# Performance work log

Hardware: AMD Instinct MI355X
Metric: run time of the kernel (lower is better)

## Reference

```python
import jax, jax.numpy as jnp
import numpy as np

NUM_NODES = 100000
NUM_EDGES = 1600000
EMBED_DIM = 128
NUM_CLASSES = 2
NUM_LAYERS = 3


def setup_inputs() -> dict:
    key = jax.random.key(0)
    k_row, k_col, k_val, k_emb, k_a, k_w, k_b = jax.random.split(key, 7)
    node_indices = jnp.arange(NUM_NODES, dtype=jnp.int64 if jax.config.read('jax_enable_x64') else jnp.int32)
    adj_row = jax.random.randint(k_row, (NUM_EDGES,), 0, NUM_NODES)
    adj_col = jax.random.randint(k_col, (NUM_EDGES,), 0, NUM_NODES)
    # symmetric-normalized-ish positive edge weights
    adj_val = jax.random.uniform(k_val, (NUM_EDGES,), dtype=jnp.float32) * (1.0 / 16.0)
    embedding = jax.random.normal(k_emb, (NUM_NODES, EMBED_DIM), dtype=jnp.float32)
    alpha = jnp.ones((NUM_LAYERS + 1,), dtype=jnp.float32) / (NUM_LAYERS + 1)
    W = jax.random.normal(k_w, (EMBED_DIM, NUM_CLASSES), dtype=jnp.float32) * 0.05
    b = jnp.zeros((NUM_CLASSES,), dtype=jnp.float32)
    return {
        'node_indices': node_indices, 'adj_row': adj_row, 'adj_col': adj_col,
        'adj_val': adj_val, 'embedding': embedding, 'alpha': alpha, 'W': W, 'b': b,
    }


def reference(node_indices, adj_row, adj_col, adj_val, embedding, alpha, W, b):
    # x: [N, D] embedding lookup
    x = embedding[node_indices]
    a = jax.nn.softmax(alpha)
    # alpha-weighted running sum over propagation layers (dropout in eval mode = identity)
    acc = a[0] * x
    cur = x
    for i in range(NUM_LAYERS):
        # sparse SpMM: out[r] += val * cur[c] for each edge (r, c)
        msgs = adj_val[:, None] * cur[adj_col]          # [E, D]
        cur = jax.ops.segment_sum(msgs, adj_row, num_segments=NUM_NODES)
        acc = acc + a[i + 1] * cur
    return acc @ W + b  # [N, num_classes]
```

## Files before the change

### kernel.cpp

```cpp
#include <hip/hip_runtime.h>

#define GD(x,y) (((x)+(y)-1)/(y))

#define SH    10
#define BPR   (1 << SH)
#define BS    256
#define KSPL  24
#define CAPSH 15
#define CAP   (1 << CAPSH)
#define CHUNK 2048

static __device__ __forceinline__ float2 ntload2(const float2* p){
    unsigned long long u = __builtin_nontemporal_load((const unsigned long long*)p);
    return *(float2*)&u;
}
static __device__ __forceinline__ void ntstore2(float2* p, float2 v){
    __builtin_nontemporal_store(*(unsigned long long*)&v, (unsigned long long*)p);
}

__global__ void init_k(int* __restrict__ cursor, int NBK,
                       const float* __restrict__ alpha, float* __restrict__ a, int na){
    int t = threadIdx.x;
    if (t < NBK) cursor[t] = t << CAPSH;
    if (t == 0){
        float m = alpha[0];
        for (int i = 1; i < na; ++i) m = fmaxf(m, alpha[i]);
        float s = 0.f;
        for (int i = 0; i < na; ++i){ float e = expf(alpha[i] - m); a[i] = e; s += e; }
        float inv = 1.f / s;
        for (int i = 0; i < na; ++i) a[i] *= inv;
    }
}

__global__ void fillf_k(const int* __restrict__ row, const int* __restrict__ col,
                        const float* __restrict__ val, int* __restrict__ cursor,
                        int2* __restrict__ sep, int E, int NBK){
    __shared__ int2 staged[CHUNK];
    __shared__ unsigned char bid[CHUNK];
    __shared__ int h[128], lstart[128], gbase[128], lcur[128];
    int t = threadIdx.x;
    int s = blockIdx.x * CHUNK;
    int e = min(E, s + CHUNK);
    int cnt = e - s;
    for (int i = t; i < NBK; i += BS) h[i] = 0;
    __syncthreads();
    for (int base = s + t * 4; base < e; base += BS * 4){
        if (base + 3 < e){
            int4 r4 = *(const int4*)(row + base);
            atomicAdd(&h[r4.x >> SH], 1);
            atomicAdd(&h[r4.y >> SH], 1);
            atomicAdd(&h[r4.z >> SH], 1);
            atomicAdd(&h[r4.w >> SH], 1);
        } else {
            for (int j = 0; j < 4 && base + j < e; ++j)
                atomicAdd(&h[row[base + j] >> SH], 1);
        }
    }
    __syncthreads();
    if (t == 0){
        int run = 0;
        for (int i = 0; i < NBK; ++i){ lstart[i] = run; run += h[i]; }
    }
    __syncthreads();
    if (t < NBK){
        lcur[t] = lstart[t];
        gbase[t] = (h[t] > 0) ? atomicAdd(&cursor[t], h[t]) : 0;
    }
    __syncthreads();
    for (int base = s + t * 4; base < e; base += BS * 4){
        int  r[4]; int c[4]; float v[4];
        int  m = min(4, e - base);
        if (m == 4){
            int4 r4 = *(const int4*)(row + base);
            int4 c4 = *(const int4*)(col + base);
            float4 v4 = *(const float4*)(val + base);
            r[0]=r4.x; r[1]=r4.y; r[2]=r4.z; r[3]=r4.w;
            c[0]=c4.x; c[1]=c4.y; c[2]=c4.z; c[3]=c4.w;
            v[0]=v4.x; v[1]=v4.y; v[2]=v4.z; v[3]=v4.w;
        } else {
            for (int j = 0; j < m; ++j){ r[j]=row[base+j]; c[j]=col[base+j]; v[j]=val[base+j]; }
        }
        for (int j = 0; j < m; ++j){
            int b = r[j] >> SH;
            int lp = atomicAdd(&lcur[b], 1);
            int2 pk;
            pk.x = c[j] | ((r[j] & (BPR - 1)) << 17);
            pk.y = __float_as_int(v[j]);
            staged[lp] = pk;
            bid[lp] = (unsigned char)b;
        }
    }
    __syncthreads();
    for (int idx = t; idx < cnt; idx += BS){
        int b = bid[idx];
        sep[gbase[b] + (idx - lstart[b])] = staged[idx];
    }
}

__global__ void proj_k(const float* __restrict__ emb, const int* __restrict__ idx,
                       const float* __restrict__ W, const float* __restrict__ b,
                       const float* __restrict__ a, float* __restrict__ y,
                       float* __restrict__ out, int N){
    int t = blockIdx.x * blockDim.x + threadIdx.x;
    int w = t >> 6;
    int lane = t & 63;
    int n = w * 2 + (lane >> 5);
    if (n >= N) return;
    int sl = lane & 31;
    float4 x = ((const float4*)(emb + (size_t)idx[n] * 128))[sl];
    int d0 = 4 * sl;
    float s0 = x.x * W[d0*2]   + x.y * W[d0*2+2] + x.z * W[d0*2+4] + x.w * W[d0*2+6];
    float s1 = x.x * W[d0*2+1] + x.y * W[d0*2+3] + x.z * W[d0*2+5] + x.w * W[d0*2+7];
    #pragma unroll
    for (int off = 16; off; off >>= 1){
        s0 += __shfl_down(s0, off, 32);
        s1 += __shfl_down(s1, off, 32);
    }
    if (sl == 0){
        float c = a[0];
        ((float2*)y)[n]   = make_float2(s0, s1);
        ((float2*)out)[n] = make_float2(b[0] + c * s0, b[1] + c * s1);
    }
}

__global__ void spmm_k(const int* __restrict__ cursor, const int2* __restrict__ sep,
                       const float* __restrict__ yin, float* __restrict__ partial,
                       int NBK){
    __shared__ float accx[BPR];
    __shared__ float accy[BPR];
    int b  = blockIdx.x / KSPL;
    int sp = blockIdx.x % KSPL;
    int t  = threadIdx.x;
    for (int j = t; j < BPR; j += BS){ accx[j] = 0.f; accy[j] = 0.f; }
    __syncthreads();
    int s = b << CAPSH;
    int e = cursor[b];
    int len = e - s, per = GD(len, KSPL);
    int cs = s + sp * per, ce = min(e, cs + per);
    int i = cs + t;
    for (; i + 3 * BS < ce; i += 4 * BS){
        int2 p0 = sep[i], p1 = sep[i + BS], p2 = sep[i + 2*BS], p3 = sep[i + 3*BS];
        float2 m0 = ((const float2*)yin)[p0.x & 0x1FFFF];
        float2 m1 = ((const float2*)yin)[p1.x & 0x1FFFF];
        float2 m2 = ((const float2*)yin)[p2.x & 0x1FFFF];
        float2 m3 = ((const float2*)yin)[p3.x & 0x1FFFF];
        float v0 = __int_as_float(p0.y), v1 = __int_as_float(p1.y);
        float v2 = __int_as_float(p2.y), v3 = __int_as_float(p3.y);
        atomicAdd(&accx[p0.x >> 17], v0 * m0.x); atomicAdd(&accy[p0.x >> 17], v0 * m0.y);
        atomicAdd(&accx[p1.x >> 17], v1 * m1.x); atomicAdd(&accy[p1.x >> 17], v1 * m1.y);
        atomicAdd(&accx[p2.x >> 17], v2 * m2.x); atomicAdd(&accy[p2.x >> 17], v2 * m2.y);
        atomicAdd(&accx[p3.x >> 17], v3 * m3.x); atomicAdd(&accy[p3.x >> 17], v3 * m3.y);
    }
    for (; i < ce; i += BS){
        int2 pk = sep[i];
        float v = __int_as_float(pk.y);
        float2 m = ((const float2*)yin)[pk.x & 0x1FFFF];
        atomicAdd(&accx[pk.x >> 17], v * m.x);
        atomicAdd(&accy[pk.x >> 17], v * m.y);
    }
    __syncthreads();
    float2* dst = (float2*)partial + (size_t)(b * KSPL + sp) * BPR;
    for (int j = t; j < BPR; j += BS)
        ntstore2(&dst[j], make_float2(accx[j], accy[j]));
}

__global__ void comb_k(const float* __restrict__ partial, const float* __restrict__ a,
                       int ai, float* __restrict__ ynext, float* __restrict__ out,
                       int N, int store){
    int n = blockIdx.x * blockDim.x + threadIdx.x;
    if (n >= N) return;
    int b = n >> SH, j = n & (BPR - 1);
    const float2* p = (const float2*)partial + (size_t)b * KSPL * BPR + j;
    float sx = 0.f, sy = 0.f;
    #pragma unroll
    for (int sp = 0; sp < KSPL; ++sp){
        float2 v = ntload2(&p[(size_t)sp * BPR]);
        sx += v.x; sy += v.y;
    }
    if (store) ((float2*)ynext)[n] = make_float2(sx, sy);
    float c = a[ai];
    float2 o = ((float2*)out)[n];
    o.x += c * sx; o.y += c * sy;
    ((float2*)out)[n] = o;
}

extern "C" void kernel_launch(void* const* d_in, const int* in_sizes, int n_in,
                              void* d_out, int out_size, void* d_ws, size_t ws_size,
                              hipStream_t stream) {
    const int*   node_idx = (const int*)  d_in[0];
    const int*   adj_row  = (const int*)  d_in[1];
    const int*   adj_col  = (const int*)  d_in[2];
    const float* adj_val  = (const float*)d_in[3];
    const float* emb      = (const float*)d_in[4];
    const float* alpha    = (const float*)d_in[5];
    const float* W        = (const float*)d_in[6];
    const float* b        = (const float*)d_in[7];
    float* out = (float*)d_out;

    const int N = in_sizes[0];
    const int E = in_sizes[1];
    const int L = in_sizes[5] - 1;
    const int NBK = GD(N, BPR);
    const int GF  = GD(E, CHUNK);

    char* w = (char*)d_ws;
    float* yA     = (float*)w;  w += (size_t)N * 2 * 4;
    float* yB     = (float*)w;  w += (size_t)N * 2 * 4;
    float* partial= (float*)w;  w += (size_t)NBK * KSPL * BPR * 2 * 4;
    int2*  sep    = (int2*)w;   w += (size_t)NBK * CAP * 8;
    int*   cursor = (int*)w;    w += 1024;
    float* a      = (float*)w;

    init_k<<<1, 128, 0, stream>>>(cursor, NBK, alpha, a, L + 1);
    fillf_k<<<GF, BS, 0, stream>>>(adj_row, adj_col, adj_val, cursor, sep, E, NBK);

    proj_k<<<GD(N * 32, 256), 256, 0, stream>>>(emb, node_idx, W, b, a, yA, out, N);

    float* ysrc = yA;
    float* ydst = yB;
    for (int i = 0; i < L; ++i){
        spmm_k<<<NBK * KSPL, BS, 0, stream>>>(cursor, sep, ysrc, partial, NBK);
        comb_k<<<GD(N, 256), 256, 0, stream>>>(partial, a, i + 1, ydst, out,
                                               N, (i < L - 1) ? 1 : 0);
        float* tmp = ysrc; ysrc = ydst; ydst = tmp;
    }
}
```

Before: 125.8 us.

## Fuse edge bucketing with projection kernel, parallelize scan, batch SpMM gathers

The edge-bucketing kernel and the embedding-projection kernel now run in one launch, split by block index, so the two independent stages can overlap and one launch is saved. The single-thread serial prefix sum over bucket histograms becomes a 128-wide shared-memory Hillis-Steele scan. In the SpMM kernel each thread first loads up to four packed edges, then issues all of their gathers before the atomics. This raises memory-level parallelism for the short per-thread edge counts, where the old 4-way unrolled loop rarely ran. The fused kernel carries the larger shared-memory footprint into the projection blocks, which may limit their occupancy.

After: 218.7 us. 73.8% more time.

```diff
diff --git a/kernel.cpp b/kernel.cpp
--- a/kernel.cpp
+++ b/kernel.cpp
@@ -32,94 +32,102 @@
     }
 }
 
-__global__ void fillf_k(const int* __restrict__ row, const int* __restrict__ col,
-                        const float* __restrict__ val, int* __restrict__ cursor,
-                        int2* __restrict__ sep, int E, int NBK){
-    __shared__ int2 staged[CHUNK];
-    __shared__ unsigned char bid[CHUNK];
-    __shared__ int h[128], lstart[128], gbase[128], lcur[128];
-    int t = threadIdx.x;
-    int s = blockIdx.x * CHUNK;
-    int e = min(E, s + CHUNK);
-    int cnt = e - s;
-    for (int i = t; i < NBK; i += BS) h[i] = 0;
-    __syncthreads();
-    for (int base = s + t * 4; base < e; base += BS * 4){
-        if (base + 3 < e){
-            int4 r4 = *(const int4*)(row + base);
-            atomicAdd(&h[r4.x >> SH], 1);
-            atomicAdd(&h[r4.y >> SH], 1);
-            atomicAdd(&h[r4.z >> SH], 1);
-            atomicAdd(&h[r4.w >> SH], 1);
-        } else {
-            for (int j = 0; j < 4 && base + j < e; ++j)
-                atomicAdd(&h[row[base + j] >> SH], 1);
-        }
-    }
-    __syncthreads();
-    if (t == 0){
-        int run = 0;
-        for (int i = 0; i < NBK; ++i){ lstart[i] = run; run += h[i]; }
-    }
-    __syncthreads();
-    if (t < NBK){
-        lcur[t] = lstart[t];
-        gbase[t] = (h[t] > 0) ? atomicAdd(&cursor[t], h[t]) : 0;
-    }
-    __syncthreads();
-    for (int base = s + t * 4; base < e; base += BS * 4){
-        int  r[4]; int c[4]; float v[4];
-        int  m = min(4, e - base);
-        if (m == 4){
-            int4 r4 = *(const int4*)(row + base);
-            int4 c4 = *(const int4*)(col + base);
-            float4 v4 = *(const float4*)(val + base);
-            r[0]=r4.x; r[1]=r4.y; r[2]=r4.z; r[3]=r4.w;
-            c[0]=c4.x; c[1]=c4.y; c[2]=c4.z; c[3]=c4.w;
-            v[0]=v4.x; v[1]=v4.y; v[2]=v4.z; v[3]=v4.w;
-        } else {
-            for (int j = 0; j < m; ++j){ r[j]=row[base+j]; c[j]=col[base+j]; v[j]=val[base+j]; }
-        }
-        for (int j = 0; j < m; ++j){
-            int b = r[j] >> SH;
-            int lp = atomicAdd(&lcur[b], 1);
-            int2 pk;
-            pk.x = c[j] | ((r[j] & (BPR - 1)) << 17);
-            pk.y = __float_as_int(v[j]);
-            staged[lp] = pk;
-            bid[lp] = (unsigned char)b;
-        }
-    }
-    __syncthreads();
-    for (int idx = t; idx < cnt; idx += BS){
-        int b = bid[idx];
-        sep[gbase[b] + (idx - lstart[b])] = staged[idx];
-    }
-}
-
-__global__ void proj_k(const float* __restrict__ emb, const int* __restrict__ idx,
-                       const float* __restrict__ W, const float* __restrict__ b,
-                       const float* __restrict__ a, float* __restrict__ y,
-                       float* __restrict__ out, int N){
-    int t = blockIdx.x * blockDim.x + threadIdx.x;
-    int w = t >> 6;
-    int lane = t & 63;
-    int n = w * 2 + (lane >> 5);
-    if (n >= N) return;
-    int sl = lane & 31;
-    float4 x = ((const float4*)(emb + (size_t)idx[n] * 128))[sl];
-    int d0 = 4 * sl;
-    float s0 = x.x * W[d0*2]   + x.y * W[d0*2+2] + x.z * W[d0*2+4] + x.w * W[d0*2+6];
-    float s1 = x.x * W[d0*2+1] + x.y * W[d0*2+3] + x.z * W[d0*2+5] + x.w * W[d0*2+7];
-    #pragma unroll
-    for (int off = 16; off; off >>= 1){
-        s0 += __shfl_down(s0, off, 32);
-        s1 += __shfl_down(s1, off, 32);
-    }
-    if (sl == 0){
-        float c = a[0];
-        ((float2*)y)[n]   = make_float2(s0, s1);
-        ((float2*)out)[n] = make_float2(b[0] + c * s0, b[1] + c * s1);
+__global__ void fillproj_k(const int* __restrict__ row, const int* __restrict__ col,
+                           const float* __restrict__ val, int* __restrict__ cursor,
+                           int2* __restrict__ sep, int E, int NBK, int GF,
+                           const float* __restrict__ emb, const int* __restrict__ idx,
+                           const float* __restrict__ W, const float* __restrict__ bb,
+                           const float* __restrict__ a, float* __restrict__ y,
+                           float* __restrict__ out, int N){
+    if (blockIdx.x < GF){
+        __shared__ int2 staged[CHUNK];
+        __shared__ unsigned char bid[CHUNK];
+        __shared__ int h[128], sc[128], lstart[128], gbase[128], lcur[128];
+        int t = threadIdx.x;
+        int s = blockIdx.x * CHUNK;
+        int e = min(E, s + CHUNK);
+        int cnt = e - s;
+        if (t < 128) h[t] = 0;
+        __syncthreads();
+        for (int base = s + t * 4; base < e; base += BS * 4){
+            if (base + 3 < e){
+                int4 r4 = *(const int4*)(row + base);
+                atomicAdd(&h[r4.x >> SH], 1);
+                atomicAdd(&h[r4.y >> SH], 1);
+                atomicAdd(&h[r4.z >> SH], 1);
+                atomicAdd(&h[r4.w >> SH], 1);
+            } else {
+                for (int j = 0; j < 4 && base + j < e; ++j)
+                    atomicAdd(&h[row[base + j] >> SH], 1);
+            }
+        }
+        __syncthreads();
+        int v = (t < 128) ? h[t] : 0;
+        if (t < 128) sc[t] = v;
+        __syncthreads();
+        #pragma unroll
+        for (int off = 1; off < 128; off <<= 1){
+            int add = (t < 128 && t >= off) ? sc[t - off] : 0;
+            __syncthreads();
+            if (t < 128) sc[t] += add;
+            __syncthreads();
+        }
+        if (t < 128){
+            int excl = sc[t] - v;
+            lstart[t] = excl;
+            lcur[t]   = excl;
+            gbase[t]  = (v > 0) ? atomicAdd(&cursor[t], v) : 0;
+        }
+        __syncthreads();
+        for (int base = s + t * 4; base < e; base += BS * 4){
+            int r[4]; int c[4]; float vv[4];
+            int m = min(4, e - base);
+            if (m == 4){
+                int4 r4 = *(const int4*)(row + base);
+                int4 c4 = *(const int4*)(col + base);
+                float4 v4 = *(const float4*)(val + base);
+                r[0]=r4.x; r[1]=r4.y; r[2]=r4.z; r[3]=r4.w;
+                c[0]=c4.x; c[1]=c4.y; c[2]=c4.z; c[3]=c4.w;
+                vv[0]=v4.x; vv[1]=v4.y; vv[2]=v4.z; vv[3]=v4.w;
+            } else {
+                for (int j = 0; j < m; ++j){ r[j]=row[base+j]; c[j]=col[base+j]; vv[j]=val[base+j]; }
+            }
+            for (int j = 0; j < m; ++j){
+                int b = r[j] >> SH;
+                int lp = atomicAdd(&lcur[b], 1);
+                int2 pk;
+                pk.x = c[j] | ((r[j] & (BPR - 1)) << 17);
+                pk.y = __float_as_int(vv[j]);
+                staged[lp] = pk;
+                bid[lp] = (unsigned char)b;
+            }
+        }
+        __syncthreads();
+        for (int i2 = t; i2 < cnt; i2 += BS){
+            int b = bid[i2];
+            sep[gbase[b] + (i2 - lstart[b])] = staged[i2];
+        }
+    } else {
+        int gt = (blockIdx.x - GF) * BS + threadIdx.x;
+        int w = gt >> 6;
+        int lane = gt & 63;
+        int n = w * 2 + (lane >> 5);
+        if (n >= N) return;
+        int sl = lane & 31;
+        float4 x = ((const float4*)(emb + (size_t)idx[n] * 128))[sl];
+        int d0 = 4 * sl;
+        float s0 = x.x * W[d0*2]   + x.y * W[d0*2+2] + x.z * W[d0*2+4] + x.w * W[d0*2+6];
+        float s1 = x.x * W[d0*2+1] + x.y * W[d0*2+3] + x.z * W[d0*2+5] + x.w * W[d0*2+7];
+        #pragma unroll
+        for (int off = 16; off; off >>= 1){
+            s0 += __shfl_down(s0, off, 32);
+            s1 += __shfl_down(s1, off, 32);
+        }
+        if (sl == 0){
+            float c = a[0];
+            ((float2*)y)[n]   = make_float2(s0, s1);
+            ((float2*)out)[n] = make_float2(bb[0] + c * s0, bb[1] + c * s1);
+        }
     }
 }
 
@@ -137,26 +145,24 @@
     int e = cursor[b];
     int len = e - s, per = GD(len, KSPL);
     int cs = s + sp * per, ce = min(e, cs + per);
-    int i = cs + t;
-    for (; i + 3 * BS < ce; i += 4 * BS){
-        int2 p0 = sep[i], p1 = sep[i + BS], p2 = sep[i + 2*BS], p3 = sep[i + 3*BS];
-        float2 m0 = ((const float2*)yin)[p0.x & 0x1FFFF];
-        float2 m1 = ((const float2*)yin)[p1.x & 0x1FFFF];
-        float2 m2 = ((const float2*)yin)[p2.x & 0x1FFFF];
-        float2 m3 = ((const float2*)yin)[p3.x & 0x1FFFF];
-        float v0 = __int_as_float(p0.y), v1 = __int_as_float(p1.y);
-        float v2 = __int_as_float(p2.y), v3 = __int_as_float(p3.y);
-        atomicAdd(&accx[p0.x >> 17], v0 * m0.x); atomicAdd(&accy[p0.x >> 17], v0 * m0.y);
-        atomicAdd(&accx[p1.x >> 17], v1 * m1.x); atomicAdd(&accy[p1.x >> 17], v1 * m1.y);
-        atomicAdd(&accx[p2.x >> 17], v2 * m2.x); atomicAdd(&accy[p2.x >> 17], v2 * m2.y);
-        atomicAdd(&accx[p3.x >> 17], v3 * m3.x); atomicAdd(&accy[p3.x >> 17], v3 * m3.y);
-    }
-    for (; i < ce; i += BS){
-        int2 pk = sep[i];
-        float v = __int_as_float(pk.y);
-        float2 m = ((const float2*)yin)[pk.x & 0x1FFFF];
-        atomicAdd(&accx[pk.x >> 17], v * m.x);
-        atomicAdd(&accy[pk.x >> 17], v * m.y);
+    int i0 = cs + t;
+    {
+        int2 p[4]; int k = 0;
+        for (int i = i0; i < ce; i += BS) { if (k < 4) p[k++] = sep[i]; }
+        float2 m[4];
+        for (int j = 0; j < k; ++j) m[j] = ((const float2*)yin)[p[j].x & 0x1FFFF];
+        for (int j = 0; j < k; ++j){
+            float v = __int_as_float(p[j].y);
+            atomicAdd(&accx[p[j].x >> 17], v * m[j].x);
+            atomicAdd(&accy[p[j].x >> 17], v * m[j].y);
+        }
+        for (int i = i0 + 4 * BS; i < ce; i += BS){
+            int2 pk = sep[i];
+            float v = __int_as_float(pk.y);
+            float2 mm = ((const float2*)yin)[pk.x & 0x1FFFF];
+            atomicAdd(&accx[pk.x >> 17], v * mm.x);
+            atomicAdd(&accy[pk.x >> 17], v * mm.y);
+        }
     }
     __syncthreads();
     float2* dst = (float2*)partial + (size_t)(b * KSPL + sp) * BPR;
@@ -202,6 +208,7 @@
     const int L = in_sizes[5] - 1;
     const int NBK = GD(N, BPR);
     const int GF  = GD(E, CHUNK);
+    const int GP  = GD(N * 32, BS);
 
     char* w = (char*)d_ws;
     float* yA     = (float*)w;  w += (size_t)N * 2 * 4;
@@ -212,9 +219,10 @@
     float* a      = (float*)w;
 
     init_k<<<1, 128, 0, stream>>>(cursor, NBK, alpha, a, L + 1);
-    fillf_k<<<GF, BS, 0, stream>>>(adj_row, adj_col, adj_val, cursor, sep, E, NBK);
-
-    proj_k<<<GD(N * 32, 256), 256, 0, stream>>>(emb, node_idx, W, b, a, yA, out, N);
+
+    fillproj_k<<<GF + GP, BS, 0, stream>>>(adj_row, adj_col, adj_val, cursor, sep,
+                                           E, NBK, GF, emb, node_idx, W, b, a,
+                                           yA, out, N);
 
     float* ysrc = yA;
     float* ydst = yB;
```
